# Optimization experiments

Measured on AMD Instinct MI355X. Metric: run time of the kernel, lower is better.

The kernel has to match this reference:

```python
import jax, jax.numpy as jnp
import numpy as np

N = 100000            # number of pose-graph nodes (keyframes)
E = 2000000           # number of edges (last one is the 'key' edge)
KEY_EDGE_WEIGHT = 0.1 # default key_edge_weight in forward
_EPS2 = 1e-8          # small-angle threshold on squared norms
_TINY = 1e-12

# quaternion layout follows pypose: [x, y, z, w]; SE3 7-vec is [t(3), q(4)]

def _quat_to_mat(q):
    x, y, z, w = q[..., 0], q[..., 1], q[..., 2], q[..., 3]
    xx, yy, zz = x * x, y * y, z * z
    xy, xz, yz = x * y, x * z, y * z
    wx, wy, wz = w * x, w * y, w * z
    R = jnp.stack([
        jnp.stack([1 - 2 * (yy + zz), 2 * (xy - wz), 2 * (xz + wy)], -1),
        jnp.stack([2 * (xy + wz), 1 - 2 * (xx + zz), 2 * (yz - wx)], -1),
        jnp.stack([2 * (xz - wy), 2 * (yz + wx), 1 - 2 * (xx + yy)], -1),
    ], -2)
    return R  # [...,3,3]

def _mat_to_tq(M):
    """mat2SE3: [...,4,4] -> (t [...,3], q [...,4] xyzw). Branchless copysign method."""
    R = M[..., :3, :3]
    t = M[..., :3, 3]
    m00, m11, m22 = R[..., 0, 0], R[..., 1, 1], R[..., 2, 2]
    qw = 0.5 * jnp.sqrt(jnp.clip(1 + m00 + m11 + m22, _TINY))
    sx = jnp.where(R[..., 2, 1] - R[..., 1, 2] >= 0, 1.0, -1.0)
    sy = jnp.where(R[..., 0, 2] - R[..., 2, 0] >= 0, 1.0, -1.0)
    sz = jnp.where(R[..., 1, 0] - R[..., 0, 1] >= 0, 1.0, -1.0)
    qx = sx * 0.5 * jnp.sqrt(jnp.clip(1 + m00 - m11 - m22, _TINY))
    qy = sy * 0.5 * jnp.sqrt(jnp.clip(1 - m00 + m11 - m22, _TINY))
    qz = sz * 0.5 * jnp.sqrt(jnp.clip(1 - m00 - m11 + m22, _TINY))
    return t, jnp.stack([qx, qy, qz, qw], -1)

def _qmul(q1, q2):
    v1, w1 = q1[..., :3], q1[..., 3:]
    v2, w2 = q2[..., :3], q2[..., 3:]
    w = w1 * w2 - jnp.sum(v1 * v2, -1, keepdims=True)
    v = w1 * v2 + w2 * v1 + jnp.cross(v1, v2)
    return jnp.concatenate([v, w], -1)

def _qrot(q, v):
    qv, w = q[..., :3], q[..., 3:]
    return v + 2.0 * jnp.cross(qv, jnp.cross(qv, v) + w * v)

def _so3_log(q):
    """unit quaternion -> rotation vector phi [...,3]."""
    s = jnp.where(q[..., 3:] < 0, -1.0, 1.0)  # canonical hemisphere (w>=0)
    v, w = s * q[..., :3], (s * q[..., 3:])[..., 0]
    n2 = jnp.sum(v * v, -1)
    n = jnp.sqrt(jnp.clip(n2, _TINY))
    big = 2.0 * jnp.arctan2(n, w) / n
    small = 2.0 / w - 2.0 * n2 / (3.0 * w ** 3)
    scale = jnp.where(n2 > _EPS2, big, small)
    return scale[..., None] * v

def _se3_log(t, q):
    """SE3 Log map -> [tau(3), phi(3)] (pypose se3 ordering)."""
    phi = _so3_log(q)
    th2 = jnp.sum(phi * phi, -1)
    th = jnp.sqrt(jnp.clip(th2, _TINY))
    half = 0.5 * th
    sin_half = jnp.where(th2 > _EPS2, jnp.sin(half), 1.0)
    coef_big = (1.0 - half * jnp.cos(half) / sin_half) / jnp.clip(th2, _TINY)
    coef = jnp.where(th2 > _EPS2, coef_big, 1.0 / 12.0 + th2 / 720.0)
    pxt = jnp.cross(phi, t)
    tau = t - 0.5 * pxt + coef[..., None] * jnp.cross(phi, pxt)
    return jnp.concatenate([tau, phi], -1)

def setup_inputs() -> dict:
    key = jax.random.key(0)
    k1, k2, k3, k4, k5 = jax.random.split(key, 5)
    # node SE3 params: random unit quats + translations -> [N,7]
    qn = jax.random.normal(k1, (N, 4), jnp.float32)
    qn = qn / jnp.linalg.norm(qn, axis=-1, keepdims=True)
    tn = jax.random.normal(k2, (N, 3), jnp.float32)
    nodes = jnp.concatenate([tn, qn], -1)
    edges = jax.random.randint(k3, (E, 2), 0, N, dtype=jnp.int64)
    # measurement poses as valid 4x4 SE3 matrices [E,4,4]
    qe = jax.random.normal(k4, (E, 4), jnp.float32)
    qe = qe / jnp.linalg.norm(qe, axis=-1, keepdims=True)
    te = jax.random.normal(k5, (E, 3), jnp.float32)
    top = jnp.concatenate([_quat_to_mat(qe), te[..., None]], -1)   # [E,3,4]
    bottom = jnp.broadcast_to(jnp.array([0.0, 0.0, 0.0, 1.0], jnp.float32), (E, 1, 4))
    poses = jnp.concatenate([top, bottom], -2)
    return {"nodes": nodes, "poses": poses, "edges": edges}

def reference(nodes, poses, edges):
    # nodes_all = cat([poses_SE3[0:1] (frozen), nodes[1:]])
    nodes_all = jnp.concatenate([jax.lax.stop_gradient(nodes[:1]), nodes[1:]], 0)
    n1 = nodes_all[edges[:, 0]]
    n2 = nodes_all[edges[:, 1]]
    t1, q1 = n1[:, :3], n1[:, 3:]
    t2, q2 = n2[:, :3], n2[:, 3:]
    # rel = node1.Inv() @ node2
    q1i = jnp.concatenate([-q1[:, :3], q1[:, 3:]], -1)
    t12 = _qrot(q1i, t2 - t1)
    q12 = _qmul(q1i, q2)
    # error = mat2SE3(poses) @ rel
    tp, qp = _mat_to_tq(poses)
    te_ = tp + _qrot(qp, t12)
    qe_ = _qmul(qp, q12)
    err = _se3_log(te_, qe_)  # [E,6]
    # last edge is the key edge, scaled by key_edge_weight (same math as the
    # original's split-then-concat, done with one vectorized pass + row weight)
    w = jnp.concatenate([jnp.ones((E - 1,), err.dtype),
                         jnp.full((1,), KEY_EDGE_WEIGHT, err.dtype)])
    return err * w[:, None]
```

## Files before the change

kernel.cpp:

```cpp
#include <hip/hip_runtime.h>

#define K_EPS2 1e-8f
#define K_TINY 1e-12f
#define KEY_EDGE_WEIGHT 0.1f

typedef float uf4 __attribute__((ext_vector_type(4), aligned(4)));

__device__ __forceinline__ float3 f3(float x, float y, float z) { return make_float3(x, y, z); }
__device__ __forceinline__ float3 add3(float3 a, float3 b) { return f3(a.x + b.x, a.y + b.y, a.z + b.z); }
__device__ __forceinline__ float3 sub3(float3 a, float3 b) { return f3(a.x - b.x, a.y - b.y, a.z - b.z); }
__device__ __forceinline__ float3 scl3(float s, float3 a) { return f3(s * a.x, s * a.y, s * a.z); }
__device__ __forceinline__ float dot3(float3 a, float3 b) { return a.x * b.x + a.y * b.y + a.z * b.z; }
__device__ __forceinline__ float3 cross3(float3 a, float3 b) {
    return f3(a.y * b.z - a.z * b.y,
              a.z * b.x - a.x * b.z,
              a.x * b.y - a.y * b.x);
}

__device__ __forceinline__ float3 qrot(float3 qv, float qw, float3 v) {
    float3 t = add3(cross3(qv, v), scl3(qw, v));
    return add3(v, scl3(2.0f, cross3(qv, t)));
}

__device__ __forceinline__ void qmul(float3 v1, float w1, float3 v2, float w2,
                                     float3* v, float* w) {
    *w = w1 * w2 - dot3(v1, v2);
    *v = add3(add3(scl3(w1, v2), scl3(w2, v1)), cross3(v1, v2));
}

__global__ __launch_bounds__(256) void PoseGraph_kernel(
    const float* __restrict__ nodes,
    const float* __restrict__ poses,
    const int*   __restrict__ edges,
    float*       __restrict__ out,
    int E) {
    int e = blockIdx.x * blockDim.x + threadIdx.x;
    if (e >= E) return;

    int2 ij = *(const int2*)(edges + (size_t)2 * e);

    const float* pa = nodes + (size_t)7 * ij.x;
    const float* pb = nodes + (size_t)7 * ij.y;
    uf4 a0 = *(const uf4*)(pa);
    uf4 a1 = *(const uf4*)(pa + 3);
    uf4 b0 = *(const uf4*)(pb);
    uf4 b1 = *(const uf4*)(pb + 3);

    float3 t1  = f3(a0.x, a0.y, a0.z);
    float3 q1v = f3(a1.x, a1.y, a1.z);
    float  q1w = a1.w;
    float3 t2  = f3(b0.x, b0.y, b0.z);
    float3 q2v = f3(b1.x, b1.y, b1.z);
    float  q2w = b1.w;

    const float4* p4 = (const float4*)(poses + (size_t)e * 16);
    float4 r0 = p4[0];
    float4 r1 = p4[1];
    float4 r2 = p4[2];

    float3 q1iv = f3(-q1v.x, -q1v.y, -q1v.z);
    float3 t12 = qrot(q1iv, q1w, sub3(t2, t1));
    float3 q12v; float q12w;
    qmul(q1iv, q1w, q2v, q2w, &q12v, &q12w);

    float m00 = r0.x, m01 = r0.y, m02 = r0.z;
    float m10 = r1.x, m11 = r1.y, m12 = r1.z;
    float m20 = r2.x, m21 = r2.y, m22 = r2.z;
    float3 tp = f3(r0.w, r1.w, r2.w);

    float qpw = 0.5f * sqrtf(fmaxf(1.0f + m00 + m11 + m22, K_TINY));
    float qpx = ((m21 - m12 >= 0.0f) ? 0.5f : -0.5f) * sqrtf(fmaxf(1.0f + m00 - m11 - m22, K_TINY));
    float qpy = ((m02 - m20 >= 0.0f) ? 0.5f : -0.5f) * sqrtf(fmaxf(1.0f - m00 + m11 - m22, K_TINY));
    float qpz = ((m10 - m01 >= 0.0f) ? 0.5f : -0.5f) * sqrtf(fmaxf(1.0f - m00 - m11 + m22, K_TINY));
    float3 qpv = f3(qpx, qpy, qpz);

    float3 te = add3(tp, qrot(qpv, qpw, t12));
    float3 qev; float qew;
    qmul(qpv, qpw, q12v, q12w, &qev, &qew);

    float s = (qew < 0.0f) ? -1.0f : 1.0f;
    float3 v = scl3(s, qev);
    float w = s * qew;
    float nn2 = dot3(v, v);
    float scale;
    if (nn2 > K_EPS2) {
        float n = sqrtf(nn2);
        scale = 2.0f * atan2f(n, w) / n;
    } else {
        scale = 2.0f / w - 2.0f * nn2 / (3.0f * w * w * w);
    }
    float3 phi = scl3(scale, v);

    float th2 = dot3(phi, phi);
    float coef;
    if (th2 > K_EPS2) {
        float th = sqrtf(th2);
        float half = 0.5f * th;
        float sh = sinf(half);
        float ch = cosf(half);
        coef = (1.0f - half * ch / sh) / th2;
    } else {
        coef = 1.0f / 12.0f + th2 / 720.0f;
    }
    float3 pxt = cross3(phi, te);
    float3 tau = add3(sub3(te, scl3(0.5f, pxt)), scl3(coef, cross3(phi, pxt)));

    float wgt = (e == E - 1) ? KEY_EDGE_WEIGHT : 1.0f;

    float* o = out + (size_t)6 * e;
    *(float2*)(o + 0) = make_float2(tau.x * wgt, tau.y * wgt);
    *(float2*)(o + 2) = make_float2(tau.z * wgt, phi.x * wgt);
    *(float2*)(o + 4) = make_float2(phi.y * wgt, phi.z * wgt);
}

extern "C" void kernel_launch(void* const* d_in, const int* in_sizes, int n_in,
                              void* d_out, int out_size, void* d_ws, size_t ws_size,
                              hipStream_t stream) {
    const float* nodes = (const float*)d_in[0];
    const float* poses = (const float*)d_in[1];
    const int*   edges = (const int*)d_in[2];
    float* out = (float*)d_out;

    int E = in_sizes[2] / 2;
    int threads = 256;
    int blocks = (E + threads - 1) / threads;
    PoseGraph_kernel<<<blocks, threads, 0, stream>>>(nodes, poses, edges, out, E);
}
```

Baseline: 62.47 us.

## Use persistent grid-stride loop with software-prefetched edge, node and pose loads

```diff
diff --git a/kernel.cpp b/kernel.cpp
--- a/kernel.cpp
+++ b/kernel.cpp
@@ -3,8 +3,6 @@
 #define K_EPS2 1e-8f
 #define K_TINY 1e-12f
 #define KEY_EDGE_WEIGHT 0.1f
-
-typedef float uf4 __attribute__((ext_vector_type(4), aligned(4)));
 
 __device__ __forceinline__ float3 f3(float x, float y, float z) { return make_float3(x, y, z); }
 __device__ __forceinline__ float3 add3(float3 a, float3 b) { return f3(a.x + b.x, a.y + b.y, a.z + b.z); }
@@ -28,40 +26,31 @@
     *v = add3(add3(scl3(w1, v2), scl3(w2, v1)), cross3(v1, v2));
 }
 
-__global__ __launch_bounds__(256) void PoseGraph_kernel(
-    const float* __restrict__ nodes,
-    const float* __restrict__ poses,
-    const int*   __restrict__ edges,
-    float*       __restrict__ out,
-    int E) {
-    int e = blockIdx.x * blockDim.x + threadIdx.x;
-    if (e >= E) return;
+struct NP {
+    float3 t1, q1v, t2, q2v;
+    float  q1w, q2w;
+};
 
-    int2 ij = *(const int2*)(edges + (size_t)2 * e);
-
+__device__ __forceinline__ NP load_nodes(const float* __restrict__ nodes, int2 ij) {
     const float* pa = nodes + (size_t)7 * ij.x;
     const float* pb = nodes + (size_t)7 * ij.y;
-    uf4 a0 = *(const uf4*)(pa);
-    uf4 a1 = *(const uf4*)(pa + 3);
-    uf4 b0 = *(const uf4*)(pb);
-    uf4 b1 = *(const uf4*)(pb + 3);
+    NP n;
+    n.t1  = f3(pa[0], pa[1], pa[2]);
+    n.q1v = f3(pa[3], pa[4], pa[5]);
+    n.q1w = pa[6];
+    n.t2  = f3(pb[0], pb[1], pb[2]);
+    n.q2v = f3(pb[3], pb[4], pb[5]);
+    n.q2w = pb[6];
+    return n;
+}
 
-    float3 t1  = f3(a0.x, a0.y, a0.z);
-    float3 q1v = f3(a1.x, a1.y, a1.z);
-    float  q1w = a1.w;
-    float3 t2  = f3(b0.x, b0.y, b0.z);
-    float3 q2v = f3(b1.x, b1.y, b1.z);
-    float  q2w = b1.w;
-
-    const float4* p4 = (const float4*)(poses + (size_t)e * 16);
-    float4 r0 = p4[0];
-    float4 r1 = p4[1];
-    float4 r2 = p4[2];
-
-    float3 q1iv = f3(-q1v.x, -q1v.y, -q1v.z);
-    float3 t12 = qrot(q1iv, q1w, sub3(t2, t1));
+__device__ __forceinline__ void compute_store(
+    float* __restrict__ out, int e, int E,
+    const NP& n, float4 r0, float4 r1, float4 r2) {
+    float3 q1iv = f3(-n.q1v.x, -n.q1v.y, -n.q1v.z);
+    float3 t12 = qrot(q1iv, n.q1w, sub3(n.t2, n.t1));
     float3 q12v; float q12w;
-    qmul(q1iv, q1w, q2v, q2w, &q12v, &q12w);
+    qmul(q1iv, n.q1w, n.q2v, n.q2w, &q12v, &q12w);
 
     float m00 = r0.x, m01 = r0.y, m02 = r0.z;
     float m10 = r1.x, m11 = r1.y, m12 = r1.z;
@@ -84,8 +73,8 @@
     float nn2 = dot3(v, v);
     float scale;
     if (nn2 > K_EPS2) {
-        float n = sqrtf(nn2);
-        scale = 2.0f * atan2f(n, w) / n;
+        float nrm = sqrtf(nn2);
+        scale = 2.0f * atan2f(nrm, w) / nrm;
     } else {
         scale = 2.0f / w - 2.0f * nn2 / (3.0f * w * w * w);
     }
@@ -113,6 +102,48 @@
     *(float2*)(o + 4) = make_float2(phi.y * wgt, phi.z * wgt);
 }
 
+__global__ __launch_bounds__(256) void PoseGraph_kernel(
+    const float* __restrict__ nodes,
+    const float* __restrict__ poses,
+    const int*   __restrict__ edges,
+    float*       __restrict__ out,
+    int E) {
+    const int S = gridDim.x * blockDim.x;
+    int e = blockIdx.x * blockDim.x + threadIdx.x;
+    if (e >= E) return;
+
+    int2 ij = *(const int2*)(edges + (size_t)2 * e);
+    const float4* p4 = (const float4*)(poses + (size_t)e * 16);
+    float4 r0 = p4[0];
+    float4 r1 = p4[1];
+    float4 r2 = p4[2];
+    NP cur = load_nodes(nodes, ij);
+
+    int e1 = e + S;
+    int2 ij1 = ij;
+    if (e1 < E) ij1 = *(const int2*)(edges + (size_t)2 * e1);
+
+    while (e1 < E) {
+        NP nxt = load_nodes(nodes, ij1);
+        const float4* q4 = (const float4*)(poses + (size_t)e1 * 16);
+        float4 s0 = q4[0];
+        float4 s1 = q4[1];
+        float4 s2 = q4[2];
+
+        int e2 = e1 + S;
+        int2 ij2 = ij1;
+        if (e2 < E) ij2 = *(const int2*)(edges + (size_t)2 * e2);
+
+        compute_store(out, e, E, cur, r0, r1, r2);
+
+        cur = nxt;
+        r0 = s0; r1 = s1; r2 = s2;
+        e = e1; e1 = e2; ij1 = ij2;
+    }
+
+    compute_store(out, e, E, cur, r0, r1, r2);
+}
+
 extern "C" void kernel_launch(void* const* d_in, const int* in_sizes, int n_in,
                               void* d_out, int out_size, void* d_ws, size_t ws_size,
                               hipStream_t stream) {
@@ -123,6 +154,8 @@
 
     int E = in_sizes[2] / 2;
     int threads = 256;
-    int blocks = (E + threads - 1) / threads;
+    int blocks = 2048;
+    int max_blocks = (E + threads - 1) / threads;
+    if (blocks > max_blocks) blocks = max_blocks;
     PoseGraph_kernel<<<blocks, threads, 0, stream>>>(nodes, poses, edges, out, E);
 }
```

After: 52.29 us. -16.3%, faster.

## Replace atan2/sincos with polynomial approximations and use a grid-stride loop

Applied to the files above, without the earlier changes.

```diff
diff --git a/kernel.cpp b/kernel.cpp
--- a/kernel.cpp
+++ b/kernel.cpp
@@ -1,10 +1,7 @@
 #include <hip/hip_runtime.h>
 
-#define K_EPS2 1e-8f
 #define K_TINY 1e-12f
 #define KEY_EDGE_WEIGHT 0.1f
-
-typedef float uf4 __attribute__((ext_vector_type(4), aligned(4)));
 
 __device__ __forceinline__ float3 f3(float x, float y, float z) { return make_float3(x, y, z); }
 __device__ __forceinline__ float3 add3(float3 a, float3 b) { return f3(a.x + b.x, a.y + b.y, a.z + b.z); }
@@ -28,89 +25,86 @@
     *v = add3(add3(scl3(w1, v2), scl3(w2, v1)), cross3(v1, v2));
 }
 
+__device__ __forceinline__ float atan_poly01(float r) {
+    float r2 = r * r;
+    float p = fmaf(r2, 0.0208351f, -0.0851330f);
+    p = fmaf(r2, p, 0.1801410f);
+    p = fmaf(r2, p, -0.3302995f);
+    p = fmaf(r2, p, 0.9998660f);
+    return r * p;
+}
+
 __global__ __launch_bounds__(256) void PoseGraph_kernel(
     const float* __restrict__ nodes,
     const float* __restrict__ poses,
     const int*   __restrict__ edges,
     float*       __restrict__ out,
     int E) {
-    int e = blockIdx.x * blockDim.x + threadIdx.x;
-    if (e >= E) return;
+    const int stride = gridDim.x * blockDim.x;
+    for (int e = blockIdx.x * blockDim.x + threadIdx.x; e < E; e += stride) {
+        int2 ij = *(const int2*)(edges + (size_t)2 * e);
 
-    int2 ij = *(const int2*)(edges + (size_t)2 * e);
+        const float* pa = nodes + (size_t)7 * ij.x;
+        const float* pb = nodes + (size_t)7 * ij.y;
+        float3 t1  = f3(pa[0], pa[1], pa[2]);
+        float3 q1v = f3(pa[3], pa[4], pa[5]);
+        float  q1w = pa[6];
+        float3 t2  = f3(pb[0], pb[1], pb[2]);
+        float3 q2v = f3(pb[3], pb[4], pb[5]);
+        float  q2w = pb[6];
 
-    const float* pa = nodes + (size_t)7 * ij.x;
-    const float* pb = nodes + (size_t)7 * ij.y;
-    uf4 a0 = *(const uf4*)(pa);
-    uf4 a1 = *(const uf4*)(pa + 3);
-    uf4 b0 = *(const uf4*)(pb);
-    uf4 b1 = *(const uf4*)(pb + 3);
+        const float4* p4 = (const float4*)(poses + (size_t)e * 16);
+        float4 r0 = p4[0];
+        float4 r1 = p4[1];
+        float4 r2 = p4[2];
 
-    float3 t1  = f3(a0.x, a0.y, a0.z);
-    float3 q1v = f3(a1.x, a1.y, a1.z);
-    float  q1w = a1.w;
-    float3 t2  = f3(b0.x, b0.y, b0.z);
-    float3 q2v = f3(b1.x, b1.y, b1.z);
-    float  q2w = b1.w;
+        float3 q1iv = f3(-q1v.x, -q1v.y, -q1v.z);
+        float3 t12 = qrot(q1iv, q1w, sub3(t2, t1));
+        float3 q12v; float q12w;
+        qmul(q1iv, q1w, q2v, q2w, &q12v, &q12w);
 
-    const float4* p4 = (const float4*)(poses + (size_t)e * 16);
-    float4 r0 = p4[0];
-    float4 r1 = p4[1];
-    float4 r2 = p4[2];
+        float m00 = r0.x, m01 = r0.y, m02 = r0.z;
+        float m10 = r1.x, m11 = r1.y, m12 = r1.z;
+        float m20 = r2.x, m21 = r2.y, m22 = r2.z;
+        float3 tp = f3(r0.w, r1.w, r2.w);
 
-    float3 q1iv = f3(-q1v.x, -q1v.y, -q1v.z);
-    float3 t12 = qrot(q1iv, q1w, sub3(t2, t1));
-    float3 q12v; float q12w;
-    qmul(q1iv, q1w, q2v, q2w, &q12v, &q12w);
+        float qpw = 0.5f * sqrtf(fmaxf(1.0f + m00 + m11 + m22, K_TINY));
+        float qpx = ((m21 - m12 >= 0.0f) ? 0.5f : -0.5f) * sqrtf(fmaxf(1.0f + m00 - m11 - m22, K_TINY));
+        float qpy = ((m02 - m20 >= 0.0f) ? 0.5f : -0.5f) * sqrtf(fmaxf(1.0f - m00 + m11 - m22, K_TINY));
+        float qpz = ((m10 - m01 >= 0.0f) ? 0.5f : -0.5f) * sqrtf(fmaxf(1.0f - m00 - m11 + m22, K_TINY));
+        float3 qpv = f3(qpx, qpy, qpz);
 
-    float m00 = r0.x, m01 = r0.y, m02 = r0.z;
-    float m10 = r1.x, m11 = r1.y, m12 = r1.z;
-    float m20 = r2.x, m21 = r2.y, m22 = r2.z;
-    float3 tp = f3(r0.w, r1.w, r2.w);
+        float3 te = add3(tp, qrot(qpv, qpw, t12));
+        float3 qev; float qew;
+        qmul(qpv, qpw, q12v, q12w, &qev, &qew);
 
-    float qpw = 0.5f * sqrtf(fmaxf(1.0f + m00 + m11 + m22, K_TINY));
-    float qpx = ((m21 - m12 >= 0.0f) ? 0.5f : -0.5f) * sqrtf(fmaxf(1.0f + m00 - m11 - m22, K_TINY));
-    float qpy = ((m02 - m20 >= 0.0f) ? 0.5f : -0.5f) * sqrtf(fmaxf(1.0f - m00 + m11 - m22, K_TINY));
-    float qpz = ((m10 - m01 >= 0.0f) ? 0.5f : -0.5f) * sqrtf(fmaxf(1.0f - m00 - m11 + m22, K_TINY));
-    float3 qpv = f3(qpx, qpy, qpz);
+        float s = (qew < 0.0f) ? -1.0f : 1.0f;
+        float3 v = scl3(s, qev);
+        float w = s * qew;
+        float nn2 = dot3(v, v);
+        float n = sqrtf(fmaxf(nn2, K_TINY));
+        float mn = fminf(n, w), mx = fmaxf(n, w);
+        float r = mn * __builtin_amdgcn_rcpf(mx);
+        float at = atan_poly01(r);
+        float ang = (n > w) ? (1.5707963f - at) : at;
+        float scale = 2.0f * ang * __builtin_amdgcn_rcpf(n);
+        float3 phi = scl3(scale, v);
 
-    float3 te = add3(tp, qrot(qpv, qpw, t12));
-    float3 qev; float qew;
-    qmul(qpv, qpw, q12v, q12w, &qev, &qew);
+        float u = dot3(phi, phi);
+        float coef = fmaf(u, 2.0876757e-8f, 8.2671958e-7f);
+        coef = fmaf(u, coef, 3.3068783e-5f);
+        coef = fmaf(u, coef, 1.3888889e-3f);
+        coef = fmaf(u, coef, 8.3333333e-2f);
+        float3 pxt = cross3(phi, te);
+        float3 tau = add3(sub3(te, scl3(0.5f, pxt)), scl3(coef, cross3(phi, pxt)));
 
-    float s = (qew < 0.0f) ? -1.0f : 1.0f;
-    float3 v = scl3(s, qev);
-    float w = s * qew;
-    float nn2 = dot3(v, v);
-    float scale;
-    if (nn2 > K_EPS2) {
-        float n = sqrtf(nn2);
-        scale = 2.0f * atan2f(n, w) / n;
-    } else {
-        scale = 2.0f / w - 2.0f * nn2 / (3.0f * w * w * w);
+        float wgt = (e == E - 1) ? KEY_EDGE_WEIGHT : 1.0f;
+
+        float* o = out + (size_t)6 * e;
+        *(float2*)(o + 0) = make_float2(tau.x * wgt, tau.y * wgt);
+        *(float2*)(o + 2) = make_float2(tau.z * wgt, phi.x * wgt);
+        *(float2*)(o + 4) = make_float2(phi.y * wgt, phi.z * wgt);
     }
-    float3 phi = scl3(scale, v);
-
-    float th2 = dot3(phi, phi);
-    float coef;
-    if (th2 > K_EPS2) {
-        float th = sqrtf(th2);
-        float half = 0.5f * th;
-        float sh = sinf(half);
-        float ch = cosf(half);
-        coef = (1.0f - half * ch / sh) / th2;
-    } else {
-        coef = 1.0f / 12.0f + th2 / 720.0f;
-    }
-    float3 pxt = cross3(phi, te);
-    float3 tau = add3(sub3(te, scl3(0.5f, pxt)), scl3(coef, cross3(phi, pxt)));
-
-    float wgt = (e == E - 1) ? KEY_EDGE_WEIGHT : 1.0f;
-
-    float* o = out + (size_t)6 * e;
-    *(float2*)(o + 0) = make_float2(tau.x * wgt, tau.y * wgt);
-    *(float2*)(o + 2) = make_float2(tau.z * wgt, phi.x * wgt);
-    *(float2*)(o + 4) = make_float2(phi.y * wgt, phi.z * wgt);
 }
 
 extern "C" void kernel_launch(void* const* d_in, const int* in_sizes, int n_in,
@@ -123,6 +117,8 @@
 
     int E = in_sizes[2] / 2;
     int threads = 256;
-    int blocks = (E + threads - 1) / threads;
+    int blocks = 2048;
+    int max_blocks = (E + threads - 1) / threads;
+    if (blocks > max_blocks) blocks = max_blocks;
     PoseGraph_kernel<<<blocks, threads, 0, stream>>>(nodes, poses, edges, out, E);
 }
```

Result: slower. 67.38 us (+7.9%).
